# Kernel optimization log

Measured on AMD Instinct MI355X. Metric: run time of the kernel, lower is better.

## Reference

```python
import jax, jax.numpy as jnp
import numpy as np

N_NODES = 100000
N_EDGES = 1600000
IN_C, HID_C, OUT_C = 64, 64, 32


def setup_inputs() -> dict:
    key = jax.random.key(0)
    ks = jax.random.split(key, 10)
    return {
        "x": jax.random.normal(ks[0], (N_NODES, IN_C), dtype=jnp.float32),
        "edge_index": jax.random.randint(ks[1], (2, N_EDGES), 0, N_NODES, dtype=jnp.int32),
        "W_l": jax.random.normal(ks[2], (IN_C, HID_C), dtype=jnp.float32) * 0.1,
        "W_r": jax.random.normal(ks[3], (IN_C, HID_C), dtype=jnp.float32) * 0.1,
        "b1": jax.random.normal(ks[4], (HID_C,), dtype=jnp.float32) * 0.1,
        "W_g": jax.random.normal(ks[5], (HID_C, OUT_C), dtype=jnp.float32) * 0.1,
        "att_src": jax.random.normal(ks[6], (OUT_C,), dtype=jnp.float32) * 0.1,
        "att_dst": jax.random.normal(ks[7], (OUT_C,), dtype=jnp.float32) * 0.1,
        "b2": jax.random.normal(ks[8], (OUT_C,), dtype=jnp.float32) * 0.1,
    }


def _gnn(x, edge_index, W_l, W_r, b1, W_g, att_src, att_dst, b2):
    n = x.shape[0]
    src, dst = edge_index[0], edge_index[1]

    # --- SAGEConv: mean neighbor aggregation + root transform ---
    deg = jax.ops.segment_sum(jnp.ones_like(src, dtype=x.dtype), dst, num_segments=n)
    agg = jax.ops.segment_sum(x[src], dst, num_segments=n)  # [N, IN_C]
    agg = agg / jnp.maximum(deg, 1.0)[:, None]
    h = agg @ W_l + b1 + x @ W_r
    h = jax.nn.relu(h)
    # dropout(p=0.5) is identity in eval mode

    # --- GATConv (heads=1), with self-loops (PyG default) ---
    loop = jnp.arange(n, dtype=src.dtype)
    s = jnp.concatenate([src, loop])
    d = jnp.concatenate([dst, loop])
    z = h @ W_g                      # [N, OUT_C]
    a_s = z @ att_src                # [N] per-node source score
    a_d = z @ att_dst                # [N] per-node dest score
    e = jax.nn.leaky_relu(a_s[s] + a_d[d], negative_slope=0.2)  # [E+N]
    # segment softmax over edges grouped by destination node
    m = jax.ops.segment_max(e, d, num_segments=n)
    ex = jnp.exp(e - m[d])
    denom = jax.ops.segment_sum(ex, d, num_segments=n)
    alpha = ex / denom[d]
    out = jax.ops.segment_sum(alpha[:, None] * z[s], d, num_segments=n) + b2

    return jax.nn.log_softmax(out, axis=1)


def reference(x, edge_index, W_l, W_r, b1, W_g, att_src, att_dst, b2):
    return _gnn(x, edge_index, W_l, W_r, b1, W_g, att_src, att_dst, b2)
```

## Files before the change

### kernel.cpp

```cpp
#include <hip/hip_runtime.h>
#include <cstdint>
#include <cstddef>


typedef unsigned short ushort_t;
typedef unsigned int uint_t;
typedef __attribute__((ext_vector_type(8))) short short8;
typedef __attribute__((ext_vector_type(4))) float f32x4;
typedef __attribute__((ext_vector_type(2))) float f32x2;

__device__ inline ushort_t f2bf(float f) {
    uint_t u = __float_as_uint(f);
    uint_t r = (u + 0x7fffu + ((u >> 16) & 1u)) >> 16;
    return (ushort_t)r;
}

#define PART_CHUNK 16384


__global__ __launch_bounds__(256) void k_pre(const float* __restrict__ x, ushort_t* __restrict__ xh,
                                             unsigned char* __restrict__ xq,
                                             const int* __restrict__ ei, int* __restrict__ tot,
                                             const float* __restrict__ Wl, const float* __restrict__ Wr,
                                             const float* __restrict__ Wg,
                                             ushort_t* __restrict__ Wlrt, ushort_t* __restrict__ Wgt,
                                             unsigned char* __restrict__ zq,
                                             int n4, int E, int NB, int N, int nchunk) {
    __shared__ int h[512];
    int bid = blockIdx.x, tid = threadIdx.x;
    int idx = bid * 256 + tid;
    if (idx < n4) {
        float4 v = ((const float4*)x)[idx];
        ushort4 o = { f2bf(v.x), f2bf(v.y), f2bf(v.z), f2bf(v.w) };
        ((ushort4*)xh)[idx] = o;
        int r = 0;
        r = __builtin_amdgcn_cvt_pk_fp8_f32(v.x, v.y, r, false);
        r = __builtin_amdgcn_cvt_pk_fp8_f32(v.z, v.w, r, true);
        ((uint_t*)xq)[idx] = (uint_t)r;
    }
    if (bid < nchunk) {
        for (int b = tid; b < NB; b += 256) h[b] = 0;
        __syncthreads();
        int b0 = bid * PART_CHUNK;
        int b1 = min(b0 + PART_CHUNK, E);
        for (int j = b0 + tid; j < b1; j += 256) atomicAdd(&h[ei[E + j] >> 8], 1);
        __syncthreads();
        for (int b = tid; b < NB; b += 256) if (h[b]) atomicAdd(&tot[b], h[b]);
    } else if (bid == nchunk) {
        if (tid < 16) ((uint_t*)(xq + (size_t)N * 64))[tid] = 0;
        if (tid < 8)  ((uint_t*)(zq + (size_t)N * 32))[tid] = 0;
    } else if (bid >= 512 && bid < 544) {
        int t = (bid - 512) * 256 + tid;
        int n = t >> 7, k = t & 127;
        float v = (k < 64) ? Wl[k * 64 + n] : Wr[(k - 64) * 64 + n];
        Wlrt[n * 128 + k] = f2bf(v);
        if (t < 32 * 64) {
            int n2 = t >> 6, k2 = t & 63;
            Wgt[n2 * 64 + k2] = f2bf(Wg[k2 * 32 + n2]);
        }
    }
}


__global__ __launch_bounds__(256) void k_scan(const int* __restrict__ tot, int* __restrict__ base,
                                              int* __restrict__ gofs, int* __restrict__ rowptr,
                                              int NB, int E, int N) {
    __shared__ int t[256];
    int tid = threadIdx.x;
    int v0 = (2 * tid < NB) ? tot[2 * tid] : 0;
    int v1 = (2 * tid + 1 < NB) ? tot[2 * tid + 1] : 0;
    t[tid] = v0 + v1;
    __syncthreads();
    for (int off = 1; off < 256; off <<= 1) {
        int u = (tid >= off) ? t[tid - off] : 0;
        __syncthreads();
        t[tid] += u;
        __syncthreads();
    }
    int pairExcl = (tid > 0) ? t[tid - 1] : 0;
    if (2 * tid < NB)     { base[2 * tid] = pairExcl;          gofs[2 * tid] = pairExcl; }
    if (2 * tid + 1 < NB) { base[2 * tid + 1] = pairExcl + v0; gofs[2 * tid + 1] = pairExcl + v0; }
    if (tid == 0) { rowptr[N] = E; base[NB] = E; }
}


__global__ __launch_bounds__(256) void k_part(const int* __restrict__ ei, int* __restrict__ gofs,
                                              uint_t* __restrict__ pairs, int E, int NB) {
    __shared__ int h[512];
    __shared__ int ofs[512];
    int tid = threadIdx.x;
    for (int b = tid; b < NB; b += 256) h[b] = 0;
    __syncthreads();
    int b0 = blockIdx.x * PART_CHUNK;
    int b1 = min(b0 + PART_CHUNK, E);
    for (int j = b0 + tid; j < b1; j += 256) atomicAdd(&h[ei[E + j] >> 8], 1);
    __syncthreads();
    for (int b = tid; b < NB; b += 256) ofs[b] = h[b] ? atomicAdd(&gofs[b], h[b]) : 0;
    __syncthreads();
    for (int j = b0 + tid; j < b1; j += 256) {
        int d = ei[E + j], s = ei[j];
        int p = atomicAdd(&ofs[d >> 8], 1);
        pairs[p] = (uint_t)s | ((uint_t)(d & 255) << 24);
    }
}


__global__ __launch_bounds__(256) void k_csr(const uint_t* __restrict__ pairs, const int* __restrict__ base,
                                             int* __restrict__ rowptr, int* __restrict__ csr, int N) {
    __shared__ int h[256];
    __shared__ int s[256];
    int b = blockIdx.x;
    int d0 = b << 8;
    int e0 = base[b], e1 = base[b + 1];
    int tid = threadIdx.x;
    h[tid] = 0;
    __syncthreads();
    for (int j = e0 + tid; j < e1; j += 256) atomicAdd(&h[pairs[j] >> 24], 1);
    __syncthreads();
    int v = h[tid];
    s[tid] = v;
    __syncthreads();
    for (int off = 1; off < 256; off <<= 1) {
        int u = (tid >= off) ? s[tid - off] : 0;
        __syncthreads();
        s[tid] += u;
        __syncthreads();
    }
    int excl = s[tid] - v;
    if (d0 + tid < N) rowptr[d0 + tid] = e0 + excl;
    __syncthreads();
    h[tid] = e0 + excl;
    __syncthreads();
    for (int j = e0 + tid; j < e1; j += 256) {
        uint_t p = pairs[j];
        int pos = atomicAdd(&h[p >> 24], 1);
        csr[pos] = (int)(p & 0xffffffu);
    }
}


__global__ __launch_bounds__(256) void k_gather(const int* __restrict__ rowptr, const int* __restrict__ csr,
                                                const unsigned char* __restrict__ xq,
                                                ushort_t* __restrict__ aggh, int N) {
    __shared__ int scr[256];
    int tid = threadIdx.x;
    int l = tid & 15, g = tid >> 4;
    int i = blockIdx.x * 16 + g;
    if (i >= N) return;
    int r0 = rowptr[i], r1 = rowptr[i + 1];
    int sub = l >> 3, lc = l & 7;
    float dn = 1.0f / fmaxf((float)(r1 - r0), 1.0f);

    #pragma unroll
    for (int p = 0; p < 2; ++p) {
        const char* xb = (const char*)xq + p * 32 + lc * 4;
        float a0 = 0.f, a1 = 0.f, a2 = 0.f, a3 = 0.f;
        for (int bb = r0; bb < r1; bb += 16) {
            int idx = bb + l;
            int src = (idx < r1) ? csr[idx] : N;
            scr[tid] = src << 6;
            uint4 q0 = *(const uint4*)&scr[g * 16 + 0];
            uint4 q1 = *(const uint4*)&scr[g * 16 + 4];
            uint4 q2 = *(const uint4*)&scr[g * 16 + 8];
            uint4 q3 = *(const uint4*)&scr[g * 16 + 12];
#define HSTEP(oa, ob) { \
            uint_t off = sub ? (ob) : (oa); \
            uint_t u = *(const uint_t*)(xb + off); \
            f32x2 p0 = __builtin_amdgcn_cvt_pk_f32_fp8((int)u, false); \
            f32x2 p1 = __builtin_amdgcn_cvt_pk_f32_fp8((int)u, true); \
            a0 += p0.x; a1 += p0.y; a2 += p1.x; a3 += p1.y; }
            HSTEP(q0.x, q0.y) HSTEP(q0.z, q0.w)
            HSTEP(q1.x, q1.y) HSTEP(q1.z, q1.w)
            HSTEP(q2.x, q2.y) HSTEP(q2.z, q2.w)
            HSTEP(q3.x, q3.y) HSTEP(q3.z, q3.w)
#undef HSTEP
        }
        a0 += __shfl_xor(a0, 8, 64);
        a1 += __shfl_xor(a1, 8, 64);
        a2 += __shfl_xor(a2, 8, 64);
        a3 += __shfl_xor(a3, 8, 64);
        if (sub == 0) {
            ushort4 o = { f2bf(a0 * dn), f2bf(a1 * dn), f2bf(a2 * dn), f2bf(a3 * dn) };
            *(ushort4*)(aggh + (size_t)i * 64 + p * 32 + lc * 4) = o;
        }
    }
}


__global__ __launch_bounds__(256) void k_gemm(const ushort_t* __restrict__ aggh, const ushort_t* __restrict__ xh,
                                              const ushort_t* __restrict__ Wlrt, const ushort_t* __restrict__ Wgt,
                                              const float* __restrict__ b1,
                                              const float* __restrict__ att_src, const float* __restrict__ att_dst,
                                              unsigned char* __restrict__ zq, float* __restrict__ a_s,
                                              float* __restrict__ a_d, int N) {
    __shared__ ushort_t Wls[64 * 136];
    __shared__ ushort_t Wgs[32 * 72];
    __shared__ ushort_t hs[64 * 136];
    int tid = threadIdx.x;
    for (int t = tid; t < 64 * 16; t += 256) {
        int n = t >> 4, cq = t & 15;
        *(uint4*)(&Wls[n * 136 + cq * 8]) = *(const uint4*)(&Wlrt[n * 128 + cq * 8]);
    }
    for (int t = tid; t < 32 * 8; t += 256) {
        int n = t >> 3, cq = t & 7;
        *(uint4*)(&Wgs[n * 72 + cq * 8]) = *(const uint4*)(&Wgt[n * 64 + cq * 8]);
    }
    __syncthreads();

    int w = tid >> 6, lane = tid & 63;
    int c = lane & 15, quad = lane >> 4;
    int m0 = blockIdx.x * 64 + w * 16;
    int row = m0 + c;
    bool rowok = row < N;

    f32x4 acc[4] = {};
    #pragma unroll
    for (int kk = 0; kk < 4; ++kk) {
        const ushort_t* Abase = (kk < 2) ? aggh : xh;
        int koff = (kk & 1) * 32 + quad * 8;
        short8 a = {};
        if (rowok) a = *(const short8*)(Abase + (size_t)row * 64 + koff);
        #pragma unroll
        for (int nb = 0; nb < 4; ++nb) {
            short8 b = *(const short8*)(&Wls[(nb * 16 + c) * 136 + kk * 32 + quad * 8]);
            acc[nb] = __builtin_amdgcn_mfma_f32_16x16x32_bf16(a, b, acc[nb], 0, 0, 0);
        }
    }
    ushort_t* hw = &hs[w * 16 * 136];
    #pragma unroll
    for (int nb = 0; nb < 4; ++nb) {
        float bb = b1[nb * 16 + c];
        #pragma unroll
        for (int r = 0; r < 4; ++r) {
            float h = acc[nb][r] + bb;
            hw[(quad * 4 + r) * 136 + nb * 16 + c] = f2bf(fmaxf(h, 0.f));
        }
    }
    f32x4 acc2[2] = {};
    #pragma unroll
    for (int kk = 0; kk < 2; ++kk) {
        short8 a = *(const short8*)(&hw[c * 136 + kk * 32 + quad * 8]);
        #pragma unroll
        for (int nb = 0; nb < 2; ++nb) {
            short8 b = *(const short8*)(&Wgs[(nb * 16 + c) * 72 + kk * 32 + quad * 8]);
            acc2[nb] = __builtin_amdgcn_mfma_f32_16x16x32_bf16(a, b, acc2[nb], 0, 0, 0);
        }
    }
    float as0 = att_src[c], as1 = att_src[16 + c];
    float ad0 = att_dst[c], ad1 = att_dst[16 + c];
    #pragma unroll
    for (int r = 0; r < 4; ++r) {
        int grow = m0 + quad * 4 + r;
        float z0 = acc2[0][r], z1 = acc2[1][r];
        float ps = z0 * as0 + z1 * as1;
        float pd = z0 * ad0 + z1 * ad1;
        #pragma unroll
        for (int off = 8; off; off >>= 1) {
            ps += __shfl_xor(ps, off, 64);
            pd += __shfl_xor(pd, off, 64);
        }
        if (grow < N) {
            int r8 = __builtin_amdgcn_cvt_pk_fp8_f32(z0, z1, 0, false);
            unsigned char* zrow = zq + (size_t)grow * 32;
            zrow[c] = (unsigned char)(r8 & 0xff);
            zrow[16 + c] = (unsigned char)((r8 >> 8) & 0xff);
            if (c == 0) { a_s[grow] = ps; a_d[grow] = pd; }
        }
    }
}


__global__ __launch_bounds__(256) void k_gat(const unsigned char* __restrict__ zq, const float* __restrict__ a_s,
                                             const float* __restrict__ a_d, const int* __restrict__ rowptr,
                                             const int* __restrict__ csr, const float* __restrict__ b2,
                                             float* __restrict__ out, int N) {
    __shared__ uint2 scr[256];
    int tid = threadIdx.x;
    int l = tid & 15, g = tid >> 4;
    int i = blockIdx.x * 16 + g;
    if (i >= N) return;
    int r0 = rowptr[i], r1 = rowptr[i + 1];
    float adi = a_d[i], asi = a_s[i];
    const char* zb = (const char*)zq + l * 2;
    float accx = 0.f, accy = 0.f, dsum = 0.f;

    for (int bb = r0; bb < r1; bb += 16) {
        int idx = bb + l;
        bool valid = idx < r1;
        int s_l = valid ? csr[idx] : N;
        float w_l = 0.f;
        if (valid) {
            float e = a_s[s_l] + adi;
            e = fmaxf(e, 0.2f * e);
            w_l = __expf(e);
            dsum += w_l;
        }
        scr[tid] = make_uint2((uint_t)(s_l << 5), __float_as_uint(w_l));
        #pragma unroll
        for (int r = 0; r < 8; ++r) {
            uint4 q = *(const uint4*)&scr[g * 16 + r * 2];
            {
                uint_t u = *(const ushort_t*)(zb + q.x);
                f32x2 p = __builtin_amdgcn_cvt_pk_f32_fp8((int)u, false);
                float w = __uint_as_float(q.y);
                accx += w * p.x; accy += w * p.y;
            }
            {
                uint_t u = *(const ushort_t*)(zb + q.z);
                f32x2 p = __builtin_amdgcn_cvt_pk_f32_fp8((int)u, false);
                float w = __uint_as_float(q.w);
                accx += w * p.x; accy += w * p.y;
            }
        }
    }
    #pragma unroll
    for (int off = 8; off; off >>= 1) dsum += __shfl_xor(dsum, off, 64);
    float es = asi + adi; es = fmaxf(es, 0.2f * es);
    float wse = __expf(es);
    float denom = dsum + wse;
    uint_t us = *(const ushort_t*)((const char*)zq + (size_t)i * 32 + l * 2);
    f32x2 pself = __builtin_amdgcn_cvt_pk_f32_fp8((int)us, false);
    accx += wse * pself.x;
    accy += wse * pself.y;

    float rden = 1.0f / denom;
    float o0 = accx * rden + b2[l * 2];
    float o1 = accy * rden + b2[l * 2 + 1];
    float m2 = fmaxf(o0, o1);
    #pragma unroll
    for (int off = 8; off; off >>= 1) m2 = fmaxf(m2, __shfl_xor(m2, off, 64));
    float ssum = __expf(o0 - m2) + __expf(o1 - m2);
    #pragma unroll
    for (int off = 8; off; off >>= 1) ssum += __shfl_xor(ssum, off, 64);
    float lg = m2 + __logf(ssum);
    float2 r = { o0 - lg, o1 - lg };
    *(float2*)(out + (size_t)i * 32 + l * 2) = r;
}


extern "C" void kernel_launch(void* const* d_in, const int* in_sizes, int n_in,
                              void* d_out, int out_size, void* d_ws, size_t ws_size,
                              hipStream_t stream) {
    const float* x       = (const float*)d_in[0];
    const int*   ei      = (const int*)d_in[1];
    const float* Wl      = (const float*)d_in[2];
    const float* Wr      = (const float*)d_in[3];
    const float* b1      = (const float*)d_in[4];
    const float* Wg      = (const float*)d_in[5];
    const float* att_src = (const float*)d_in[6];
    const float* att_dst = (const float*)d_in[7];
    const float* b2      = (const float*)d_in[8];
    float* out = (float*)d_out;

    int N = in_sizes[0] / 64;
    int E = in_sizes[1] / 2;
    int NB = (N + 255) >> 8;

    char* ws = (char*)d_ws;
    size_t off = 0;
    auto alloc = [&](size_t bytes) { size_t r = off; off += (bytes + 255) & ~(size_t)255; return r; };
    int* tot       = (int*)(ws + alloc((size_t)(NB + 1) * 4));
    int* base      = (int*)(ws + alloc((size_t)(NB + 1) * 4));
    int* gofs      = (int*)(ws + alloc((size_t)(NB + 1) * 4));
    int* rowptr    = (int*)(ws + alloc((size_t)(N + 1) * 4));
    uint_t* pairs  = (uint_t*)(ws + alloc((size_t)E * 4));
    int* csr       = (int*)(ws + alloc((size_t)E * 4));
    ushort_t* xh   = (ushort_t*)(ws + alloc((size_t)N * 64 * 2));
    unsigned char* xq = (unsigned char*)(ws + alloc((size_t)(N + 1) * 64));
    ushort_t* aggh = (ushort_t*)(ws + alloc((size_t)N * 64 * 2));
    unsigned char* zq = (unsigned char*)(ws + alloc((size_t)(N + 1) * 32));
    float* a_s     = (float*)(ws + alloc((size_t)N * 4));
    float* a_d     = (float*)(ws + alloc((size_t)N * 4));
    ushort_t* Wlrt = (ushort_t*)(ws + alloc(64 * 128 * 2));
    ushort_t* Wgt  = (ushort_t*)(ws + alloc(32 * 64 * 2));

    (void)hipMemsetAsync(tot, 0, (size_t)NB * 4, stream);

    int nchunk = (E + PART_CHUNK - 1) / PART_CHUNK;
    int n4 = N * 64 / 4;
    int gpre = (n4 + 255) / 256;
    if (gpre < 545) gpre = 545;
    k_pre    <<<gpre, 256, 0, stream>>>(x, xh, xq, ei, tot, Wl, Wr, Wg, Wlrt, Wgt, zq, n4, E, NB, N, nchunk);
    k_scan   <<<1, 256, 0, stream>>>(tot, base, gofs, rowptr, NB, E, N);
    k_part   <<<nchunk, 256, 0, stream>>>(ei, gofs, pairs, E, NB);
    k_csr    <<<NB, 256, 0, stream>>>(pairs, base, rowptr, csr, N);
    k_gather <<<(N + 15) / 16, 256, 0, stream>>>(rowptr, csr, xq, aggh, N);
    k_gemm   <<<(N + 63) / 64, 256, 0, stream>>>(aggh, xh, Wlrt, Wgt, b1, att_src, att_dst, zq, a_s, a_d, N);
    k_gat    <<<(N + 15) / 16, 256, 0, stream>>>(zq, a_s, a_d, rowptr, csr, b2, out, N);
}
```

Before: 225.0 us.

## Widen per-lane gathers in SAGE and GAT kernels and halve partition chunk

The SAGE gather kernel now reads 8 fp8 features per lane in a single pass over the neighbour list, where it previously made two passes of 4 features each. This halves the CSR and shared-memory index traffic and the loop overhead. The GAT kernel switches to 4-byte loads, with two half-groups handling alternating edges, and combines their sums with a shuffle. Each lane then computes log-softmax over 4 outputs and writes float4. PART_CHUNK is also halved, which changes the partition granularity, and the wider accumulators raise register use.

```diff
diff --git a/kernel.cpp b/kernel.cpp
--- a/kernel.cpp
+++ b/kernel.cpp
@@ -14,8 +14,11 @@
     uint_t r = (u + 0x7fffu + ((u >> 16) & 1u)) >> 16;
     return (ushort_t)r;
 }
-
-#define PART_CHUNK 16384
+__device__ inline uint_t pkbf(float a, float b) {
+    return (uint_t)f2bf(a) | ((uint_t)f2bf(b) << 16);
+}
+
+#define PART_CHUNK 8192
 
 
 __global__ __launch_bounds__(256) void k_pre(const float* __restrict__ x, ushort_t* __restrict__ xh,
@@ -149,40 +152,41 @@
     if (i >= N) return;
     int r0 = rowptr[i], r1 = rowptr[i + 1];
     int sub = l >> 3, lc = l & 7;
-    float dn = 1.0f / fmaxf((float)(r1 - r0), 1.0f);
-
-    #pragma unroll
-    for (int p = 0; p < 2; ++p) {
-        const char* xb = (const char*)xq + p * 32 + lc * 4;
-        float a0 = 0.f, a1 = 0.f, a2 = 0.f, a3 = 0.f;
-        for (int bb = r0; bb < r1; bb += 16) {
-            int idx = bb + l;
-            int src = (idx < r1) ? csr[idx] : N;
-            scr[tid] = src << 6;
-            uint4 q0 = *(const uint4*)&scr[g * 16 + 0];
-            uint4 q1 = *(const uint4*)&scr[g * 16 + 4];
-            uint4 q2 = *(const uint4*)&scr[g * 16 + 8];
-            uint4 q3 = *(const uint4*)&scr[g * 16 + 12];
+    const char* xb = (const char*)xq + lc * 8;
+    float a0 = 0.f, a1 = 0.f, a2 = 0.f, a3 = 0.f;
+    float a4 = 0.f, a5 = 0.f, a6 = 0.f, a7 = 0.f;
+    for (int bb = r0; bb < r1; bb += 16) {
+        int idx = bb + l;
+        int src = (idx < r1) ? csr[idx] : N;
+        scr[tid] = src << 6;
+        uint4 q0 = *(const uint4*)&scr[g * 16 + 0];
+        uint4 q1 = *(const uint4*)&scr[g * 16 + 4];
+        uint4 q2 = *(const uint4*)&scr[g * 16 + 8];
+        uint4 q3 = *(const uint4*)&scr[g * 16 + 12];
 #define HSTEP(oa, ob) { \
-            uint_t off = sub ? (ob) : (oa); \
-            uint_t u = *(const uint_t*)(xb + off); \
-            f32x2 p0 = __builtin_amdgcn_cvt_pk_f32_fp8((int)u, false); \
-            f32x2 p1 = __builtin_amdgcn_cvt_pk_f32_fp8((int)u, true); \
-            a0 += p0.x; a1 += p0.y; a2 += p1.x; a3 += p1.y; }
-            HSTEP(q0.x, q0.y) HSTEP(q0.z, q0.w)
-            HSTEP(q1.x, q1.y) HSTEP(q1.z, q1.w)
-            HSTEP(q2.x, q2.y) HSTEP(q2.z, q2.w)
-            HSTEP(q3.x, q3.y) HSTEP(q3.z, q3.w)
+        uint_t off = sub ? (ob) : (oa); \
+        uint2 u = *(const uint2*)(xb + off); \
+        f32x2 p0 = __builtin_amdgcn_cvt_pk_f32_fp8((int)u.x, false); \
+        f32x2 p1 = __builtin_amdgcn_cvt_pk_f32_fp8((int)u.x, true); \
+        f32x2 p2 = __builtin_amdgcn_cvt_pk_f32_fp8((int)u.y, false); \
+        f32x2 p3 = __builtin_amdgcn_cvt_pk_f32_fp8((int)u.y, true); \
+        a0 += p0.x; a1 += p0.y; a2 += p1.x; a3 += p1.y; \
+        a4 += p2.x; a5 += p2.y; a6 += p3.x; a7 += p3.y; }
+        HSTEP(q0.x, q0.y) HSTEP(q0.z, q0.w)
+        HSTEP(q1.x, q1.y) HSTEP(q1.z, q1.w)
+        HSTEP(q2.x, q2.y) HSTEP(q2.z, q2.w)
+        HSTEP(q3.x, q3.y) HSTEP(q3.z, q3.w)
 #undef HSTEP
-        }
-        a0 += __shfl_xor(a0, 8, 64);
-        a1 += __shfl_xor(a1, 8, 64);
-        a2 += __shfl_xor(a2, 8, 64);
-        a3 += __shfl_xor(a3, 8, 64);
-        if (sub == 0) {
-            ushort4 o = { f2bf(a0 * dn), f2bf(a1 * dn), f2bf(a2 * dn), f2bf(a3 * dn) };
-            *(ushort4*)(aggh + (size_t)i * 64 + p * 32 + lc * 4) = o;
-        }
+    }
+    a0 += __shfl_xor(a0, 8, 64); a1 += __shfl_xor(a1, 8, 64);
+    a2 += __shfl_xor(a2, 8, 64); a3 += __shfl_xor(a3, 8, 64);
+    a4 += __shfl_xor(a4, 8, 64); a5 += __shfl_xor(a5, 8, 64);
+    a6 += __shfl_xor(a6, 8, 64); a7 += __shfl_xor(a7, 8, 64);
+    if (sub == 0) {
+        float dn = 1.0f / fmaxf((float)(r1 - r0), 1.0f);
+        uint4 o = { pkbf(a0 * dn, a1 * dn), pkbf(a2 * dn, a3 * dn),
+                    pkbf(a4 * dn, a5 * dn), pkbf(a6 * dn, a7 * dn) };
+        *(uint4*)(aggh + (size_t)i * 64 + lc * 8) = o;
     }
 }
 
@@ -281,8 +285,9 @@
     if (i >= N) return;
     int r0 = rowptr[i], r1 = rowptr[i + 1];
     float adi = a_d[i], asi = a_s[i];
-    const char* zb = (const char*)zq + l * 2;
-    float accx = 0.f, accy = 0.f, dsum = 0.f;
+    int sub = l >> 3, lc = l & 7;
+    const char* zb = (const char*)zq + lc * 4;
+    float a0 = 0.f, a1 = 0.f, a2 = 0.f, a3 = 0.f, dsum = 0.f;
 
     for (int bb = r0; bb < r1; bb += 16) {
         int idx = bb + l;
@@ -299,42 +304,44 @@
         #pragma unroll
         for (int r = 0; r < 8; ++r) {
             uint4 q = *(const uint4*)&scr[g * 16 + r * 2];
-            {
-                uint_t u = *(const ushort_t*)(zb + q.x);
-                f32x2 p = __builtin_amdgcn_cvt_pk_f32_fp8((int)u, false);
-                float w = __uint_as_float(q.y);
-                accx += w * p.x; accy += w * p.y;
-            }
-            {
-                uint_t u = *(const ushort_t*)(zb + q.z);
-                f32x2 p = __builtin_amdgcn_cvt_pk_f32_fp8((int)u, false);
-                float w = __uint_as_float(q.w);
-                accx += w * p.x; accy += w * p.y;
-            }
+            uint_t off = sub ? q.z : q.x;
+            float w = __uint_as_float(sub ? q.w : q.y);
+            uint_t u = *(const uint_t*)(zb + off);
+            f32x2 p0 = __builtin_amdgcn_cvt_pk_f32_fp8((int)u, false);
+            f32x2 p1 = __builtin_amdgcn_cvt_pk_f32_fp8((int)u, true);
+            a0 += w * p0.x; a1 += w * p0.y;
+            a2 += w * p1.x; a3 += w * p1.y;
         }
     }
     #pragma unroll
     for (int off = 8; off; off >>= 1) dsum += __shfl_xor(dsum, off, 64);
+    a0 += __shfl_xor(a0, 8, 64); a1 += __shfl_xor(a1, 8, 64);
+    a2 += __shfl_xor(a2, 8, 64); a3 += __shfl_xor(a3, 8, 64);
     float es = asi + adi; es = fmaxf(es, 0.2f * es);
     float wse = __expf(es);
     float denom = dsum + wse;
-    uint_t us = *(const ushort_t*)((const char*)zq + (size_t)i * 32 + l * 2);
-    f32x2 pself = __builtin_amdgcn_cvt_pk_f32_fp8((int)us, false);
-    accx += wse * pself.x;
-    accy += wse * pself.y;
+    uint_t us = *(const uint_t*)((const char*)zq + (size_t)i * 32 + lc * 4);
+    f32x2 s0 = __builtin_amdgcn_cvt_pk_f32_fp8((int)us, false);
+    f32x2 s1 = __builtin_amdgcn_cvt_pk_f32_fp8((int)us, true);
+    a0 += wse * s0.x; a1 += wse * s0.y;
+    a2 += wse * s1.x; a3 += wse * s1.y;
 
     float rden = 1.0f / denom;
-    float o0 = accx * rden + b2[l * 2];
-    float o1 = accy * rden + b2[l * 2 + 1];
-    float m2 = fmaxf(o0, o1);
-    #pragma unroll
-    for (int off = 8; off; off >>= 1) m2 = fmaxf(m2, __shfl_xor(m2, off, 64));
-    float ssum = __expf(o0 - m2) + __expf(o1 - m2);
-    #pragma unroll
-    for (int off = 8; off; off >>= 1) ssum += __shfl_xor(ssum, off, 64);
+    float o0 = a0 * rden + b2[lc * 4 + 0];
+    float o1 = a1 * rden + b2[lc * 4 + 1];
+    float o2 = a2 * rden + b2[lc * 4 + 2];
+    float o3 = a3 * rden + b2[lc * 4 + 3];
+    float m2 = fmaxf(fmaxf(o0, o1), fmaxf(o2, o3));
+    #pragma unroll
+    for (int off = 4; off; off >>= 1) m2 = fmaxf(m2, __shfl_xor(m2, off, 64));
+    float ssum = __expf(o0 - m2) + __expf(o1 - m2) + __expf(o2 - m2) + __expf(o3 - m2);
+    #pragma unroll
+    for (int off = 4; off; off >>= 1) ssum += __shfl_xor(ssum, off, 64);
     float lg = m2 + __logf(ssum);
-    float2 r = { o0 - lg, o1 - lg };
-    *(float2*)(out + (size_t)i * 32 + l * 2) = r;
+    if (sub == 0) {
+        float4 r = { o0 - lg, o1 - lg, o2 - lg, o3 - lg };
+        *(float4*)(out + (size_t)i * 32 + lc * 4) = r;
+    }
 }
 
 
```

After: 203.6 us. 1.11x faster.
